# Performance work log

Measured on AMD Instinct MI355X. Metric: run time of the kernel, lower is better.

## Reference

```python
import jax, jax.numpy as jnp
import numpy as np

DIM = 384
NUM_HEADS = 6
HEAD_DIM = DIM // NUM_HEADS
SCALE = HEAD_DIM ** -0.5


def setup_inputs() -> dict:
    key = jax.random.key(0)
    k_x, k_wqkv, k_bqkv, k_wp, k_bp = jax.random.split(key, 5)
    B, N, D = 16, 1024, DIM
    s = 0.02
    return {
        "x": jax.random.normal(k_x, (B, N, D), dtype=jnp.float32),
        "w_qkv": jax.random.normal(k_wqkv, (D, 3 * D), dtype=jnp.float32) * s,
        "b_qkv": jax.random.normal(k_bqkv, (3 * D,), dtype=jnp.float32) * s,
        "w_proj": jax.random.normal(k_wp, (D, D), dtype=jnp.float32) * s,
        "b_proj": jax.random.normal(k_bp, (D,), dtype=jnp.float32) * s,
    }


def reference(x, w_qkv, b_qkv, w_proj, b_proj):
    b, n, d = x.shape
    qkv = x @ w_qkv + b_qkv                               # (B, N, 3D)
    qkv = qkv.reshape(b, n, 3, NUM_HEADS, HEAD_DIM)
    qkv = jnp.transpose(qkv, (2, 0, 3, 1, 4))             # (3, B, H, N, hd)
    q, k, v = qkv[0], qkv[1], qkv[2]
    attn = jnp.einsum("bhqd,bhkd->bhqk", q, k) * SCALE    # (B, H, N, N)
    attn = jax.nn.softmax(attn, axis=-1)
    out = jnp.einsum("bhqk,bhkd->bhqd", attn, v)          # (B, H, N, hd)
    out = jnp.transpose(out, (0, 2, 1, 3)).reshape(b, n, d)
    return out @ w_proj + b_proj
```

## Files before the change

### kernel.cpp

```cpp
#include <hip/hip_runtime.h>

typedef __attribute__((ext_vector_type(8))) short short8;
typedef __attribute__((ext_vector_type(4))) float float4_t;
typedef __attribute__((ext_vector_type(4))) unsigned int uint4_t;

#define MFMA16(A, B, C) __builtin_amdgcn_mfma_f32_16x16x32_bf16(A, B, C, 0, 0, 0)

#define QSCALE 0.1803368801111168f

__device__ __forceinline__ unsigned short f2bf(float f) {
  unsigned int u = __builtin_bit_cast(unsigned int, f);
  u += 0x7FFFu + ((u >> 16) & 1u);
  return (unsigned short)(u >> 16);
}

__device__ __forceinline__ void gload16(const unsigned short* g, unsigned short* l) {
  __builtin_amdgcn_global_load_lds(
      (const __attribute__((address_space(1))) unsigned int*)(g),
      (__attribute__((address_space(3))) unsigned int*)(l), 16, 0, 0);
}

__global__ __launch_bounds__(256) void prep(
    const float* __restrict__ x, const float* __restrict__ w_qkv,
    const float* __restrict__ w_proj, unsigned short* __restrict__ xb,
    unsigned short* __restrict__ wqkvT, unsigned short* __restrict__ wprojT) {
  __shared__ unsigned short tile[32][33];
  const int bid = blockIdx.x, tid = threadIdx.x;
  if (bid < 6144) {
    const int i = bid * 256 + tid;
    float4 v = reinterpret_cast<const float4*>(x)[i];
    ushort4 r;
    r.x = f2bf(v.x); r.y = f2bf(v.y); r.z = f2bf(v.z); r.w = f2bf(v.w);
    reinterpret_cast<ushort4*>(xb)[i] = r;
    return;
  }
  const float* w; unsigned short* wT; int E, t;
  if (bid < 6576) { t = bid - 6144; w = w_qkv; wT = wqkvT; E = 1152; }
  else            { t = bid - 6576; w = w_proj; wT = wprojT; E = 384; }
  const int tiles_e = E >> 5;
  const int td = t / tiles_e, te = t - td * tiles_e;
  const int r = tid >> 3, c4 = (tid & 7) * 4;
  float4 v = *reinterpret_cast<const float4*>(&w[(size_t)(td * 32 + r) * E + te * 32 + c4]);
  tile[r][c4 + 0] = f2bf(v.x);
  tile[r][c4 + 1] = f2bf(v.y);
  tile[r][c4 + 2] = f2bf(v.z);
  tile[r][c4 + 3] = f2bf(v.w);
  __syncthreads();
  ushort4 o;
  o.x = tile[c4 + 0][r]; o.y = tile[c4 + 1][r];
  o.z = tile[c4 + 2][r]; o.w = tile[c4 + 3][r];
  *reinterpret_cast<ushort4*>(&wT[(size_t)(te * 32 + r) * 384 + td * 32 + c4]) = o;
}

__global__ __launch_bounds__(256, 2) void gemm_qkv(
    const unsigned short* __restrict__ xb,
    const unsigned short* __restrict__ wT,
    const float* __restrict__ bias,
    unsigned short* __restrict__ qb,
    unsigned short* __restrict__ kb,
    unsigned short* __restrict__ vt) {
  __shared__ alignas(16) char smem[65536];
  const int tid = threadIdx.x;
  const int wg = (blockIdx.x & 7) * 144 + (blockIdx.x >> 3);
  const int bm = wg / 9, bn = wg - bm * 9;
  const int m0 = bm * 128, n0 = bn * 128;
  const int lane = tid & 63, wid = tid >> 6;
  const int lr = lane & 15, lg = lane >> 4;
  const int wm = wid >> 1, wn = wid & 1;
  float4_t acc[4][4] = {};

  const unsigned short* asrc[4];
  const unsigned short* bsrc[4];
  int dstoff[4];
#pragma unroll
  for (int i = 0; i < 4; ++i) {
    const int idx = tid + i * 256;
    const int r = idx >> 3, c8 = idx & 7;
    const int cc = (c8 ^ (r & 7)) * 8;
    asrc[i] = xb + (size_t)(m0 + r) * 384 + cc;
    bsrc[i] = wT + (size_t)(n0 + r) * 384 + cc;
    dstoff[i] = idx * 16;
  }
  const int rxor = (lr & 7) << 4;

#pragma unroll
  for (int i = 0; i < 4; ++i) {
    gload16(asrc[i], (unsigned short*)(smem + dstoff[i]));
    gload16(bsrc[i], (unsigned short*)(smem + 32768 + dstoff[i]));
  }
  __syncthreads();

#pragma unroll
  for (int kt = 0; kt < 6; ++kt) {
    const int cur = kt & 1;
    if (kt < 5) {
      const int nb = (cur ^ 1) * 16384;
#pragma unroll
      for (int i = 0; i < 4; ++i) {
        gload16(asrc[i] + (kt + 1) * 64, (unsigned short*)(smem + nb + dstoff[i]));
        gload16(bsrc[i] + (kt + 1) * 64, (unsigned short*)(smem + 32768 + nb + dstoff[i]));
      }
    }
    const char* Ab = smem + cur * 16384;
    const char* Bb = smem + 32768 + cur * 16384;
#pragma unroll
    for (int kk = 0; kk < 2; ++kk) {
      short8 a[4], b[4];
#pragma unroll
      for (int f = 0; f < 4; ++f) {
        a[f] = *reinterpret_cast<const short8*>(
            Ab + (wm * 64 + f * 16 + lr) * 128 + ((kk * 64 + lg * 16) ^ rxor));
        b[f] = *reinterpret_cast<const short8*>(
            Bb + (wn * 64 + f * 16 + lr) * 128 + ((kk * 64 + lg * 16) ^ rxor));
      }
      if (bn < 6) {
#pragma unroll
        for (int mf = 0; mf < 4; ++mf)
#pragma unroll
          for (int nf = 0; nf < 4; ++nf)
            acc[mf][nf] = MFMA16(b[nf], a[mf], acc[mf][nf]);
      } else {
#pragma unroll
        for (int mf = 0; mf < 4; ++mf)
#pragma unroll
          for (int nf = 0; nf < 4; ++nf)
            acc[mf][nf] = MFMA16(a[mf], b[nf], acc[mf][nf]);
      }
    }
    __syncthreads();
  }

  if (bn < 6) {
    const int whichk = (bn >= 3);
    unsigned short* dst = whichk ? kb : qb;
    const float sc = whichk ? 1.f : QSCALE;
#pragma unroll
    for (int nf = 0; nf < 4; ++nf) {
      const int e0 = n0 + wn * 64 + nf * 16 + lg * 4;
      const int d0 = e0 - whichk * 384;
      const int h = d0 >> 6, hi0 = d0 & 63;
      const float4 bv4 = *reinterpret_cast<const float4*>(&bias[e0]);
#pragma unroll
      for (int mf = 0; mf < 4; ++mf) {
        const int mm = m0 + wm * 64 + mf * 16 + lr;
        const int b0 = mm >> 10, n_b = mm & 1023;
        const size_t bhh = (size_t)(b0 * 6 + h);
        ushort4 sv;
        sv.x = f2bf((acc[mf][nf][0] + bv4.x) * sc);
        sv.y = f2bf((acc[mf][nf][1] + bv4.y) * sc);
        sv.z = f2bf((acc[mf][nf][2] + bv4.z) * sc);
        sv.w = f2bf((acc[mf][nf][3] + bv4.w) * sc);
        *reinterpret_cast<ushort4*>(&dst[bhh * 65536 + (size_t)n_b * 64 + hi0]) = sv;
      }
    }
  } else {
#pragma unroll
    for (int nf = 0; nf < 4; ++nf) {
      const int e = n0 + wn * 64 + nf * 16 + lr;
      const float bv = bias[e];
      const int d = e - 768;
      const int h = d >> 6, hi = d & 63;
#pragma unroll
      for (int mf = 0; mf < 4; ++mf) {
        const int mm0 = m0 + wm * 64 + mf * 16 + lg * 4;
        const int b0 = mm0 >> 10, n_b = mm0 & 1023;
        const size_t bhh = (size_t)(b0 * 6 + h);
        const int np = (n_b & ~31) | ((n_b & 12) << 1) | ((n_b & 16) >> 2);
        ushort4 sv;
        sv.x = f2bf(acc[mf][nf][0] + bv);
        sv.y = f2bf(acc[mf][nf][1] + bv);
        sv.z = f2bf(acc[mf][nf][2] + bv);
        sv.w = f2bf(acc[mf][nf][3] + bv);
        *reinterpret_cast<ushort4*>(&vt[bhh * 65536 + (size_t)hi * 1024 + np]) = sv;
      }
    }
  }
}

__global__ __launch_bounds__(512, 6) void attn(
    const unsigned short* __restrict__ qb,
    const unsigned short* __restrict__ kb,
    const unsigned short* __restrict__ vt,
    unsigned short* __restrict__ ab) {
  __shared__ alignas(16) char smem[32768];
  const int tid = threadIdx.x;
  const int wg = (blockIdx.x & 7) * 96 + (blockIdx.x >> 3);
  const int bh = wg >> 3, qt = wg & 7;
  const int lane = tid & 63, wid = tid >> 6;
  const int lr = lane & 15, lg = lane >> 4;
  const size_t base = (size_t)bh * 65536;
  const unsigned short* qp = qb + base;
  const unsigned short* kp = kb + base;
  const unsigned short* vp = vt + base;
  const int q0 = qt * 128 + wid * 16;

  short8 aq0 = *reinterpret_cast<const short8*>(&qp[(size_t)(q0 + lr) * 64 + lg * 8]);
  short8 aq1 = *reinterpret_cast<const short8*>(&qp[(size_t)(q0 + lr) * 64 + 32 + lg * 8]);

  const int rr = tid >> 3;
  const int cc = (((tid & 7) * 16) ^ ((rr & 7) << 4)) >> 1;
  const unsigned short* ksrc = kp + rr * 64 + cc;
  const unsigned short* vsrc = vp + rr * 1024 + cc;
  unsigned short* kdst = (unsigned short*)(smem + tid * 16);
  unsigned short* vdst = (unsigned short*)(smem + 16384 + tid * 16);

  const int xr = (lr & 7) << 4;

  float lsum = 0.f;
  float4_t o[4] = {};

  gload16(ksrc, kdst);
  gload16(vsrc, vdst);
  __syncthreads();

  for (int kt = 0; kt < 16; ++kt) {
    const int cur = kt & 1;
    if (kt < 15) {
      const int nb = (cur ^ 1) * 8192;
      gload16(ksrc + (kt + 1) * 4096, (unsigned short*)(smem + nb + tid * 16));
      gload16(vsrc + (kt + 1) * 64, (unsigned short*)(smem + 16384 + nb + tid * 16));
    }
    const char* kbase = smem + cur * 8192;
    const char* vbase = smem + 16384 + cur * 8192;

#pragma unroll
    for (int half = 0; half < 2; ++half) {
      short8 bk00 = *reinterpret_cast<const short8*>(
          kbase + (half * 32 + lr) * 128 + ((lg * 16) ^ xr));
      short8 bk01 = *reinterpret_cast<const short8*>(
          kbase + (half * 32 + lr) * 128 + ((64 + lg * 16) ^ xr));
      short8 bk10 = *reinterpret_cast<const short8*>(
          kbase + (half * 32 + 16 + lr) * 128 + ((lg * 16) ^ xr));
      short8 bk11 = *reinterpret_cast<const short8*>(
          kbase + (half * 32 + 16 + lr) * 128 + ((64 + lg * 16) ^ xr));
      float4_t s0 = {}, s1 = {};
      s0 = MFMA16(bk00, aq0, s0);
      s0 = MFMA16(bk01, aq1, s0);
      s1 = MFMA16(bk10, aq0, s1);
      s1 = MFMA16(bk11, aq1, s1);

      unsigned int dw0, dw1, dw2, dw3;
      {
        const float p0 = __builtin_amdgcn_exp2f(s0[0]);
        const float p1 = __builtin_amdgcn_exp2f(s0[1]);
        const float p2 = __builtin_amdgcn_exp2f(s0[2]);
        const float p3 = __builtin_amdgcn_exp2f(s0[3]);
        asm("v_cvt_pk_bf16_f32 %0, %1, %2" : "=v"(dw0) : "v"(p0), "v"(p1));
        asm("v_cvt_pk_bf16_f32 %0, %1, %2" : "=v"(dw1) : "v"(p2), "v"(p3));
        const float p4 = __builtin_amdgcn_exp2f(s1[0]);
        const float p5 = __builtin_amdgcn_exp2f(s1[1]);
        const float p6 = __builtin_amdgcn_exp2f(s1[2]);
        const float p7 = __builtin_amdgcn_exp2f(s1[3]);
        asm("v_cvt_pk_bf16_f32 %0, %1, %2" : "=v"(dw2) : "v"(p4), "v"(p5));
        asm("v_cvt_pk_bf16_f32 %0, %1, %2" : "=v"(dw3) : "v"(p6), "v"(p7));
      }
      lsum += __builtin_bit_cast(float, dw0 << 16) +
              __builtin_bit_cast(float, dw0 & 0xFFFF0000u) +
              __builtin_bit_cast(float, dw1 << 16) +
              __builtin_bit_cast(float, dw1 & 0xFFFF0000u) +
              __builtin_bit_cast(float, dw2 << 16) +
              __builtin_bit_cast(float, dw2 & 0xFFFF0000u) +
              __builtin_bit_cast(float, dw3 << 16) +
              __builtin_bit_cast(float, dw3 & 0xFFFF0000u);

      uint4_t pw;
      pw[0] = dw0; pw[1] = dw1; pw[2] = dw2; pw[3] = dw3;
      const short8 pa = __builtin_bit_cast(short8, pw);
#pragma unroll
      for (int f = 0; f < 4; ++f) {
        short8 bv = *reinterpret_cast<const short8*>(
            vbase + (f * 16 + lr) * 128 + ((half * 64 + lg * 16) ^ xr));
        o[f] = MFMA16(pa, bv, o[f]);
      }
    }
    __syncthreads();
  }

  float t = lsum;
  t += __shfl_xor(t, 16);
  t += __shfl_xor(t, 32);
  const float inv = 1.f / t;

  const int b = bh / 6, h = bh - b * 6;
  float invj[4];
#pragma unroll
  for (int j = 0; j < 4; ++j)
    invj[j] = __shfl(inv, lg * 4 + j);
#pragma unroll
  for (int f = 0; f < 4; ++f)
#pragma unroll
    for (int j = 0; j < 4; ++j) {
      const int q = q0 + lg * 4 + j;
      ab[(size_t)(b * 1024 + q) * 384 + h * 64 + f * 16 + lr] =
          f2bf(o[f][j] * invj[j]);
    }
}

__global__ __launch_bounds__(256, 3) void gemm_proj(
    const unsigned short* __restrict__ ab,
    const unsigned short* __restrict__ wT,
    const float* __restrict__ bias,
    float* __restrict__ out) {
  __shared__ alignas(16) char smem[49152];
  const int tid = threadIdx.x;
  const int wg = (blockIdx.x & 7) * 96 + (blockIdx.x >> 3);
  const int bm = wg / 3, bn = wg - bm * 3;
  const int m0 = bm * 64, n0 = bn * 128;
  const int lane = tid & 63, wid = tid >> 6;
  const int lr = lane & 15, lg = lane >> 4;
  const int wm = wid >> 1, wn = wid & 1;
  float4_t acc[2][4] = {};

  const unsigned short* asrc[2];
  const unsigned short* bsrc[4];
  int adst[2], bdst[4];
#pragma unroll
  for (int i = 0; i < 2; ++i) {
    const int idx = tid + i * 256;
    const int r = idx >> 3, c8 = idx & 7;
    asrc[i] = ab + (size_t)(m0 + r) * 384 + (c8 ^ (r & 7)) * 8;
    adst[i] = idx * 16;
  }
#pragma unroll
  for (int i = 0; i < 4; ++i) {
    const int idx = tid + i * 256;
    const int r = idx >> 3, c8 = idx & 7;
    bsrc[i] = wT + (size_t)(n0 + r) * 384 + (c8 ^ (r & 7)) * 8;
    bdst[i] = idx * 16;
  }
  const int rxor = (lr & 7) << 4;

#pragma unroll
  for (int i = 0; i < 2; ++i) gload16(asrc[i], (unsigned short*)(smem + adst[i]));
#pragma unroll
  for (int i = 0; i < 4; ++i) gload16(bsrc[i], (unsigned short*)(smem + 16384 + bdst[i]));
  __syncthreads();

#pragma unroll
  for (int kt = 0; kt < 6; ++kt) {
    const int cur = kt & 1;
    if (kt < 5) {
#pragma unroll
      for (int i = 0; i < 2; ++i)
        gload16(asrc[i] + (kt + 1) * 64, (unsigned short*)(smem + (cur ^ 1) * 8192 + adst[i]));
#pragma unroll
      for (int i = 0; i < 4; ++i)
        gload16(bsrc[i] + (kt + 1) * 64, (unsigned short*)(smem + 16384 + (cur ^ 1) * 16384 + bdst[i]));
    }
    const char* Ab = smem + cur * 8192;
    const char* Bb = smem + 16384 + cur * 16384;
#pragma unroll
    for (int kk = 0; kk < 2; ++kk) {
      short8 a[2], b[4];
#pragma unroll
      for (int f = 0; f < 2; ++f)
        a[f] = *reinterpret_cast<const short8*>(
            Ab + (wm * 32 + f * 16 + lr) * 128 + ((kk * 64 + lg * 16) ^ rxor));
#pragma unroll
      for (int f = 0; f < 4; ++f)
        b[f] = *reinterpret_cast<const short8*>(
            Bb + (wn * 64 + f * 16 + lr) * 128 + ((kk * 64 + lg * 16) ^ rxor));
#pragma unroll
      for (int mf = 0; mf < 2; ++mf)
#pragma unroll
        for (int nf = 0; nf < 4; ++nf)
          acc[mf][nf] = MFMA16(b[nf], a[mf], acc[mf][nf]);
    }
    __syncthreads();
  }

#pragma unroll
  for (int nf = 0; nf < 4; ++nf) {
    const int e0 = n0 + wn * 64 + nf * 16 + lg * 4;
    const float4 bv4 = *reinterpret_cast<const float4*>(&bias[e0]);
#pragma unroll
    for (int mf = 0; mf < 2; ++mf) {
      const int mm = m0 + wm * 32 + mf * 16 + lr;
      float4 ov;
      ov.x = acc[mf][nf][0] + bv4.x;
      ov.y = acc[mf][nf][1] + bv4.y;
      ov.z = acc[mf][nf][2] + bv4.z;
      ov.w = acc[mf][nf][3] + bv4.w;
      *reinterpret_cast<float4*>(&out[(size_t)mm * 384 + e0]) = ov;
    }
  }
}

extern "C" void kernel_launch(void* const* d_in, const int* in_sizes, int n_in,
                              void* d_out, int out_size, void* d_ws, size_t ws_size,
                              hipStream_t stream) {
  const float* x      = (const float*)d_in[0];
  const float* w_qkv  = (const float*)d_in[1];
  const float* b_qkv  = (const float*)d_in[2];
  const float* w_proj = (const float*)d_in[3];
  const float* b_proj = (const float*)d_in[4];
  float* out = (float*)d_out;

  char* ws = (char*)d_ws;
  unsigned short* xb     = (unsigned short*)(ws);
  unsigned short* wqkvT  = (unsigned short*)(ws + 12582912);
  unsigned short* wprojT = (unsigned short*)(ws + 13467648);
  unsigned short* qb     = (unsigned short*)(ws + 13762560);
  unsigned short* kb     = (unsigned short*)(ws + 26345472);
  unsigned short* vt     = (unsigned short*)(ws + 38928384);
  unsigned short* ab     = xb;

  prep<<<6720, 256, 0, stream>>>(x, w_qkv, w_proj, xb, wqkvT, wprojT);
  gemm_qkv<<<1152, 256, 0, stream>>>(xb, wqkvT, b_qkv, qb, kb, vt);
  attn<<<768, 512, 0, stream>>>(qb, kb, vt, ab);
  gemm_proj<<<768, 256, 0, stream>>>(ab, wprojT, b_proj, out);
}
```

Before: 87.17 us.

## Shrink QKV GEMM tile to 128x64 and prioritize MFMA issue in attention

The QKV projection GEMM moves from 128x128 tiles to 128x64 tiles. That doubles the grid to 2304 workgroups, cuts shared memory to 48 KB and raises the launch bound to 3 waves per SIMD, aiming for higher occupancy and better load balance across CUs. In the attention kernel the MFMA groups are wrapped in s_setprio raises, V fragment loads are hoisted ahead of the PV MFMAs, and the row-sum accumulation is restructured as a tree to shorten the dependency chain. The cost is less reuse per tile in the GEMM, since each A tile is loaded twice as often.

```diff
diff --git a/kernel.cpp b/kernel.cpp
--- a/kernel.cpp
+++ b/kernel.cpp
@@ -52,91 +52,98 @@
   *reinterpret_cast<ushort4*>(&wT[(size_t)(te * 32 + r) * 384 + td * 32 + c4]) = o;
 }
 
-__global__ __launch_bounds__(256, 2) void gemm_qkv(
+__global__ __launch_bounds__(256, 3) void gemm_qkv(
     const unsigned short* __restrict__ xb,
     const unsigned short* __restrict__ wT,
     const float* __restrict__ bias,
     unsigned short* __restrict__ qb,
     unsigned short* __restrict__ kb,
     unsigned short* __restrict__ vt) {
-  __shared__ alignas(16) char smem[65536];
+  __shared__ alignas(16) char smem[49152];
   const int tid = threadIdx.x;
-  const int wg = (blockIdx.x & 7) * 144 + (blockIdx.x >> 3);
-  const int bm = wg / 9, bn = wg - bm * 9;
-  const int m0 = bm * 128, n0 = bn * 128;
+  const int wg = (blockIdx.x & 7) * 288 + (blockIdx.x >> 3);
+  const int bm = wg / 18, bn = wg - bm * 18;
+  const int m0 = bm * 128, n0 = bn * 64;
   const int lane = tid & 63, wid = tid >> 6;
   const int lr = lane & 15, lg = lane >> 4;
   const int wm = wid >> 1, wn = wid & 1;
-  float4_t acc[4][4] = {};
+  float4_t acc[4][2] = {};
 
   const unsigned short* asrc[4];
-  const unsigned short* bsrc[4];
-  int dstoff[4];
+  const unsigned short* bsrc[2];
+  int adst[4], bdst[2];
 #pragma unroll
   for (int i = 0; i < 4; ++i) {
     const int idx = tid + i * 256;
     const int r = idx >> 3, c8 = idx & 7;
-    const int cc = (c8 ^ (r & 7)) * 8;
-    asrc[i] = xb + (size_t)(m0 + r) * 384 + cc;
-    bsrc[i] = wT + (size_t)(n0 + r) * 384 + cc;
-    dstoff[i] = idx * 16;
+    asrc[i] = xb + (size_t)(m0 + r) * 384 + (c8 ^ (r & 7)) * 8;
+    adst[i] = idx * 16;
+  }
+#pragma unroll
+  for (int i = 0; i < 2; ++i) {
+    const int idx = tid + i * 256;
+    const int r = idx >> 3, c8 = idx & 7;
+    bsrc[i] = wT + (size_t)(n0 + r) * 384 + (c8 ^ (r & 7)) * 8;
+    bdst[i] = idx * 16;
   }
   const int rxor = (lr & 7) << 4;
 
 #pragma unroll
-  for (int i = 0; i < 4; ++i) {
-    gload16(asrc[i], (unsigned short*)(smem + dstoff[i]));
-    gload16(bsrc[i], (unsigned short*)(smem + 32768 + dstoff[i]));
-  }
+  for (int i = 0; i < 4; ++i) gload16(asrc[i], (unsigned short*)(smem + adst[i]));
+#pragma unroll
+  for (int i = 0; i < 2; ++i) gload16(bsrc[i], (unsigned short*)(smem + 32768 + bdst[i]));
   __syncthreads();
 
 #pragma unroll
   for (int kt = 0; kt < 6; ++kt) {
     const int cur = kt & 1;
     if (kt < 5) {
-      const int nb = (cur ^ 1) * 16384;
-#pragma unroll
-      for (int i = 0; i < 4; ++i) {
-        gload16(asrc[i] + (kt + 1) * 64, (unsigned short*)(smem + nb + dstoff[i]));
-        gload16(bsrc[i] + (kt + 1) * 64, (unsigned short*)(smem + 32768 + nb + dstoff[i]));
-      }
+#pragma unroll
+      for (int i = 0; i < 4; ++i)
+        gload16(asrc[i] + (kt + 1) * 64,
+                (unsigned short*)(smem + (cur ^ 1) * 16384 + adst[i]));
+#pragma unroll
+      for (int i = 0; i < 2; ++i)
+        gload16(bsrc[i] + (kt + 1) * 64,
+                (unsigned short*)(smem + 32768 + (cur ^ 1) * 8192 + bdst[i]));
     }
     const char* Ab = smem + cur * 16384;
-    const char* Bb = smem + 32768 + cur * 16384;
+    const char* Bb = smem + 32768 + cur * 8192;
 #pragma unroll
     for (int kk = 0; kk < 2; ++kk) {
-      short8 a[4], b[4];
-#pragma unroll
-      for (int f = 0; f < 4; ++f) {
+      short8 a[4], b[2];
+#pragma unroll
+      for (int f = 0; f < 4; ++f)
         a[f] = *reinterpret_cast<const short8*>(
             Ab + (wm * 64 + f * 16 + lr) * 128 + ((kk * 64 + lg * 16) ^ rxor));
+#pragma unroll
+      for (int f = 0; f < 2; ++f)
         b[f] = *reinterpret_cast<const short8*>(
-            Bb + (wn * 64 + f * 16 + lr) * 128 + ((kk * 64 + lg * 16) ^ rxor));
-      }
-      if (bn < 6) {
+            Bb + (wn * 32 + f * 16 + lr) * 128 + ((kk * 64 + lg * 16) ^ rxor));
+      if (bn < 12) {
 #pragma unroll
         for (int mf = 0; mf < 4; ++mf)
 #pragma unroll
-          for (int nf = 0; nf < 4; ++nf)
+          for (int nf = 0; nf < 2; ++nf)
             acc[mf][nf] = MFMA16(b[nf], a[mf], acc[mf][nf]);
       } else {
 #pragma unroll
         for (int mf = 0; mf < 4; ++mf)
 #pragma unroll
-          for (int nf = 0; nf < 4; ++nf)
+          for (int nf = 0; nf < 2; ++nf)
             acc[mf][nf] = MFMA16(a[mf], b[nf], acc[mf][nf]);
       }
     }
     __syncthreads();
   }
 
-  if (bn < 6) {
-    const int whichk = (bn >= 3);
+  if (bn < 12) {
+    const int whichk = (bn >= 6);
     unsigned short* dst = whichk ? kb : qb;
     const float sc = whichk ? 1.f : QSCALE;
 #pragma unroll
-    for (int nf = 0; nf < 4; ++nf) {
-      const int e0 = n0 + wn * 64 + nf * 16 + lg * 4;
+    for (int nf = 0; nf < 2; ++nf) {
+      const int e0 = n0 + wn * 32 + nf * 16 + lg * 4;
       const int d0 = e0 - whichk * 384;
       const int h = d0 >> 6, hi0 = d0 & 63;
       const float4 bv4 = *reinterpret_cast<const float4*>(&bias[e0]);
@@ -155,8 +162,8 @@
     }
   } else {
 #pragma unroll
-    for (int nf = 0; nf < 4; ++nf) {
-      const int e = n0 + wn * 64 + nf * 16 + lr;
+    for (int nf = 0; nf < 2; ++nf) {
+      const int e = n0 + wn * 32 + nf * 16 + lr;
       const float bv = bias[e];
       const int d = e - 768;
       const int h = d >> 6, hi = d & 63;
@@ -234,10 +241,12 @@
       short8 bk11 = *reinterpret_cast<const short8*>(
           kbase + (half * 32 + 16 + lr) * 128 + ((64 + lg * 16) ^ xr));
       float4_t s0 = {}, s1 = {};
+      __builtin_amdgcn_s_setprio(1);
       s0 = MFMA16(bk00, aq0, s0);
       s0 = MFMA16(bk01, aq1, s0);
       s1 = MFMA16(bk10, aq0, s1);
       s1 = MFMA16(bk11, aq1, s1);
+      __builtin_amdgcn_s_setprio(0);
 
       unsigned int dw0, dw1, dw2, dw3;
       {
@@ -254,24 +263,33 @@
         asm("v_cvt_pk_bf16_f32 %0, %1, %2" : "=v"(dw2) : "v"(p4), "v"(p5));
         asm("v_cvt_pk_bf16_f32 %0, %1, %2" : "=v"(dw3) : "v"(p6), "v"(p7));
       }
-      lsum += __builtin_bit_cast(float, dw0 << 16) +
-              __builtin_bit_cast(float, dw0 & 0xFFFF0000u) +
-              __builtin_bit_cast(float, dw1 << 16) +
-              __builtin_bit_cast(float, dw1 & 0xFFFF0000u) +
-              __builtin_bit_cast(float, dw2 << 16) +
-              __builtin_bit_cast(float, dw2 & 0xFFFF0000u) +
-              __builtin_bit_cast(float, dw3 << 16) +
-              __builtin_bit_cast(float, dw3 & 0xFFFF0000u);
+      const float t0 = __builtin_bit_cast(float, dw0 << 16) +
+                       __builtin_bit_cast(float, dw0 & 0xFFFF0000u);
+      const float t1 = __builtin_bit_cast(float, dw1 << 16) +
+                       __builtin_bit_cast(float, dw1 & 0xFFFF0000u);
+      const float t2 = __builtin_bit_cast(float, dw2 << 16) +
+                       __builtin_bit_cast(float, dw2 & 0xFFFF0000u);
+      const float t3 = __builtin_bit_cast(float, dw3 << 16) +
+                       __builtin_bit_cast(float, dw3 & 0xFFFF0000u);
+      lsum += (t0 + t1) + (t2 + t3);
 
       uint4_t pw;
       pw[0] = dw0; pw[1] = dw1; pw[2] = dw2; pw[3] = dw3;
       const short8 pa = __builtin_bit_cast(short8, pw);
-#pragma unroll
-      for (int f = 0; f < 4; ++f) {
-        short8 bv = *reinterpret_cast<const short8*>(
-            vbase + (f * 16 + lr) * 128 + ((half * 64 + lg * 16) ^ xr));
-        o[f] = MFMA16(pa, bv, o[f]);
-      }
+      short8 bv0 = *reinterpret_cast<const short8*>(
+          vbase + (0 * 16 + lr) * 128 + ((half * 64 + lg * 16) ^ xr));
+      short8 bv1 = *reinterpret_cast<const short8*>(
+          vbase + (1 * 16 + lr) * 128 + ((half * 64 + lg * 16) ^ xr));
+      short8 bv2 = *reinterpret_cast<const short8*>(
+          vbase + (2 * 16 + lr) * 128 + ((half * 64 + lg * 16) ^ xr));
+      short8 bv3 = *reinterpret_cast<const short8*>(
+          vbase + (3 * 16 + lr) * 128 + ((half * 64 + lg * 16) ^ xr));
+      __builtin_amdgcn_s_setprio(1);
+      o[0] = MFMA16(pa, bv0, o[0]);
+      o[1] = MFMA16(pa, bv1, o[1]);
+      o[2] = MFMA16(pa, bv2, o[2]);
+      o[3] = MFMA16(pa, bv3, o[3]);
+      __builtin_amdgcn_s_setprio(0);
     }
     __syncthreads();
   }
@@ -406,7 +424,7 @@
   unsigned short* ab     = xb;
 
   prep<<<6720, 256, 0, stream>>>(x, w_qkv, w_proj, xb, wqkvT, wprojT);
-  gemm_qkv<<<1152, 256, 0, stream>>>(xb, wqkvT, b_qkv, qb, kb, vt);
+  gemm_qkv<<<2304, 256, 0, stream>>>(xb, wqkvT, b_qkv, qb, kb, vt);
   attn<<<768, 512, 0, stream>>>(qb, kb, vt, ab);
   gemm_proj<<<768, 256, 0, stream>>>(ab, wprojT, b_proj, out);
 }
```

Result: no change. 88.34 us (+1.3%).
